# Optimization experiments

Hardware: AMD Instinct MI355X
Metric: run time of the kernel (lower is better)

Reference implementation:

```python
import jax, jax.numpy as jnp
import numpy as np

B, S, I, H = 64, 2048, 256, 256


def setup_inputs() -> dict:
    key = jax.random.key(0)
    kx, k1, k2, k3, k4 = jax.random.split(key, 5)
    s = 1.0 / np.sqrt(H)  # torch nn.Linear default init bound
    return {
        "x": jax.random.normal(kx, (B, S, I), dtype=jnp.float32),
        "W_xh": jax.random.uniform(k1, (H, I), jnp.float32, -s, s),
        "b_xh": jax.random.uniform(k2, (H,), jnp.float32, -s, s),
        "W_hh": jax.random.uniform(k3, (H, H), jnp.float32, -s, s),
        "b_hh": jax.random.uniform(k4, (H,), jnp.float32, -s, s),
    }


def reference(x, W_xh, b_xh, W_hh, b_hh):
    # Elman RNN, recurrence=True, tanh activation.
    # Precompute input projection for all timesteps in one batched matmul: (B,S,H)
    xp = jnp.einsum('bsi,hi->bsh', x, W_xh) + b_xh
    h0 = jnp.zeros((x.shape[0], W_hh.shape[0]), dtype=x.dtype)

    def step(h, xt):  # h: (B,H), xt: (B,H) precomputed input term
        h = jnp.tanh(h @ W_hh.T + b_hh + xt)
        return h, h

    h_last, hs = jax.lax.scan(step, h0, jnp.swapaxes(xp, 0, 1))  # hs: (S,B,H)
    h_seq = jnp.swapaxes(hs, 0, 1)  # (B,S,H), matches torch permute(1,0,2)
    return h_seq, h_last[None]  # final hidden: (1,B,H)
```

## Files before the change

kernel.cpp:

```cpp
#include <hip/hip_runtime.h>
#include <cstdint>
#include <cstddef>

typedef _Float16 h2 __attribute__((ext_vector_type(2)));

#define S_LEN 2048
#define HDIM  256
#define BATCH 64

__device__ __forceinline__ float dot2f(h2 a, h2 b, float c) {
#if __has_builtin(__builtin_amdgcn_fdot2)
    return __builtin_amdgcn_fdot2(a, b, c, false);
#else
    return c + (float)a[0] * (float)b[0] + (float)a[1] * (float)b[1];
#endif
}

__device__ __forceinline__ float tanh_fast(float x) {
    return 1.0f - 2.0f / (__expf(2.0f * x) + 1.0f);
}

__global__ void __launch_bounds__(256) xp_gemm(
    const float* __restrict__ x, const float* __restrict__ Wxh,
    const float* __restrict__ bxh, float* __restrict__ out) {
    __shared__ float As[32][68];
    __shared__ float Bs[32][68];

    const int tid = threadIdx.x;
    const int tx = tid & 15;
    const int ty = tid >> 4;
    const size_t m0 = (size_t)blockIdx.x * 64;
    const int n0 = blockIdx.y * 64;

    const int r = tid >> 3;
    const int c = (tid & 7) * 4;

    float bj[4];
#pragma unroll
    for (int j = 0; j < 4; j++) bj[j] = bxh[n0 + tx * 4 + j];

    float acc[4][4] = {};

    for (int k0 = 0; k0 < 256; k0 += 32) {
        float4 a0 = *(const float4*)&x[(m0 + r) * 256 + k0 + c];
        float4 a1 = *(const float4*)&x[(m0 + r + 32) * 256 + k0 + c];
        float4 b0 = *(const float4*)&Wxh[(size_t)(n0 + r) * 256 + k0 + c];
        float4 b1 = *(const float4*)&Wxh[(size_t)(n0 + r + 32) * 256 + k0 + c];

        __syncthreads();
        As[c + 0][r] = a0.x; As[c + 1][r] = a0.y; As[c + 2][r] = a0.z; As[c + 3][r] = a0.w;
        As[c + 0][r + 32] = a1.x; As[c + 1][r + 32] = a1.y; As[c + 2][r + 32] = a1.z; As[c + 3][r + 32] = a1.w;
        Bs[c + 0][r] = b0.x; Bs[c + 1][r] = b0.y; Bs[c + 2][r] = b0.z; Bs[c + 3][r] = b0.w;
        Bs[c + 0][r + 32] = b1.x; Bs[c + 1][r + 32] = b1.y; Bs[c + 2][r + 32] = b1.z; Bs[c + 3][r + 32] = b1.w;
        __syncthreads();

#pragma unroll
        for (int kk = 0; kk < 32; kk++) {
            float4 av = *(const float4*)&As[kk][ty * 4];
            float4 bv = *(const float4*)&Bs[kk][tx * 4];
            float aa[4] = {av.x, av.y, av.z, av.w};
            float bb[4] = {bv.x, bv.y, bv.z, bv.w};
#pragma unroll
            for (int i = 0; i < 4; i++)
#pragma unroll
                for (int j = 0; j < 4; j++)
                    acc[i][j] = fmaf(aa[i], bb[j], acc[i][j]);
        }
    }

#pragma unroll
    for (int i = 0; i < 4; i++) {
        float4 o;
        o.x = acc[i][0] + bj[0];
        o.y = acc[i][1] + bj[1];
        o.z = acc[i][2] + bj[2];
        o.w = acc[i][3] + bj[3];
        *(float4*)&out[(m0 + ty * 4 + i) * 256 + n0 + tx * 4] = o;
    }
}

__global__ void __launch_bounds__(512) rnn_recur(
    const float* __restrict__ Whh, const float* __restrict__ bhh,
    float* __restrict__ out) {
    const int b = blockIdx.x;
    const int t = threadIdx.x;
    const int h = t >> 1;
    const int half = t & 1;

    h2 w[64];
    const float* wrow = Whh + (size_t)h * HDIM + half * 128;
#pragma unroll
    for (int j = 0; j < 32; j++) {
        float4 wv = *(const float4*)&wrow[4 * j];
        w[2 * j]     = h2{(_Float16)wv.x, (_Float16)wv.y};
        w[2 * j + 1] = h2{(_Float16)wv.z, (_Float16)wv.w};
    }
    const float bias = bhh[h];

    __shared__ __align__(16) _Float16 hbuf[2][HDIM];
    for (int i = t; i < HDIM; i += 512) hbuf[0][i] = (_Float16)0.f;
    __syncthreads();

    float* xprow = out + (size_t)b * S_LEN * HDIM;
    float* hlast = out + (size_t)BATCH * S_LEN * HDIM;

    int p = 0;
    float val = 0.f;
    for (int s = 0; s < S_LEN; s++) {
        float xpv = xprow[(size_t)s * HDIM + h];

        const float4* hp4 = (const float4*)&hbuf[p][half * 128];
        float a0 = 0.f, a1 = 0.f, a2 = 0.f, a3 = 0.f;
#pragma unroll
        for (int j = 0; j < 16; j++) {
            float4 vv = hp4[j];
            a0 = dot2f(w[4 * j + 0], __builtin_bit_cast(h2, vv.x), a0);
            a1 = dot2f(w[4 * j + 1], __builtin_bit_cast(h2, vv.y), a1);
            a2 = dot2f(w[4 * j + 2], __builtin_bit_cast(h2, vv.z), a2);
            a3 = dot2f(w[4 * j + 3], __builtin_bit_cast(h2, vv.w), a3);
        }
        float part = (a0 + a1) + (a2 + a3);
        part += __shfl_xor(part, 1);

        val = tanh_fast(part + bias + xpv);

        if (half) {
            xprow[(size_t)s * HDIM + h] = val;
        } else {
            hbuf[p ^ 1][h] = (_Float16)val;
        }
        p ^= 1;
        __syncthreads();
    }
    if (!half) hlast[b * HDIM + h] = val;
}

extern "C" void kernel_launch(void* const* d_in, const int* in_sizes, int n_in,
                              void* d_out, int out_size, void* d_ws, size_t ws_size,
                              hipStream_t stream) {
    const float* x   = (const float*)d_in[0];
    const float* Wxh = (const float*)d_in[1];
    const float* bxh = (const float*)d_in[2];
    const float* Whh = (const float*)d_in[3];
    const float* bhh = (const float*)d_in[4];
    float* out = (float*)d_out;

    dim3 gridA(131072 / 64, 256 / 64);
    xp_gemm<<<gridA, 256, 0, stream>>>(x, Wxh, bxh, out);
    rnn_recur<<<BATCH, 512, 0, stream>>>(Whh, bhh, out);
}
```

Baseline: 1.530 ms.

## Batch 16 sequences per workgroup and run the recurrence with MFMA

Replaces the per-sequence dot2 recurrence (64 workgroups, one batch row each) with an MFMA-based kernel. Each of 4 workgroups handles 16 batch rows and does the h·W_hh^T product with 16x16x32 f16 MFMAs, keeping the weights in registers. Input-projection values are prefetched two timesteps ahead to hide global-load latency on the serial chain. The grid shrinks to 4 workgroups, trading parallelism across CUs for matrix-core throughput; the serial chain per step may lengthen, since each step now covers 16 rows in one workgroup.

After: 2.262 ms. 47.8% more time.

```diff
diff --git a/kernel.cpp b/kernel.cpp
--- a/kernel.cpp
+++ b/kernel.cpp
@@ -2,22 +2,17 @@
 #include <cstdint>
 #include <cstddef>
 
-typedef _Float16 h2 __attribute__((ext_vector_type(2)));
+typedef _Float16 half8 __attribute__((ext_vector_type(8)));
+typedef float f32x4 __attribute__((ext_vector_type(4)));
 
 #define S_LEN 2048
 #define HDIM  256
 #define BATCH 64
-
-__device__ __forceinline__ float dot2f(h2 a, h2 b, float c) {
-#if __has_builtin(__builtin_amdgcn_fdot2)
-    return __builtin_amdgcn_fdot2(a, b, c, false);
-#else
-    return c + (float)a[0] * (float)b[0] + (float)a[1] * (float)b[1];
-#endif
-}
+#define LROW  264
 
 __device__ __forceinline__ float tanh_fast(float x) {
-    return 1.0f - 2.0f / (__expf(2.0f * x) + 1.0f);
+    float e = __expf(2.0f * x);
+    return 1.0f - 2.0f / (e + 1.0f);
 }
 
 __global__ void __launch_bounds__(256) xp_gemm(
@@ -79,60 +74,106 @@
     }
 }
 
-__global__ void __launch_bounds__(512) rnn_recur(
+__global__ void __launch_bounds__(512, 1) rnn_mfma(
     const float* __restrict__ Whh, const float* __restrict__ bhh,
     float* __restrict__ out) {
-    const int b = blockIdx.x;
+    const int wg = blockIdx.x;
     const int t = threadIdx.x;
-    const int h = t >> 1;
-    const int half = t & 1;
+    const int w = t >> 6;
+    const int l = t & 63;
+    const int c = l & 15;
+    const int g = l >> 4;
 
-    h2 w[64];
-    const float* wrow = Whh + (size_t)h * HDIM + half * 128;
+    const int n0 = w * 32 + c;
+
+    __shared__ _Float16 hls[2][16][LROW];
+
+    half8 wf[2][8];
 #pragma unroll
-    for (int j = 0; j < 32; j++) {
-        float4 wv = *(const float4*)&wrow[4 * j];
-        w[2 * j]     = h2{(_Float16)wv.x, (_Float16)wv.y};
-        w[2 * j + 1] = h2{(_Float16)wv.z, (_Float16)wv.w};
+    for (int nt = 0; nt < 2; nt++) {
+        const float* wr = Whh + (size_t)(n0 + nt * 16) * HDIM;
+#pragma unroll
+        for (int kt = 0; kt < 8; kt++) {
+            float4 u = *(const float4*)&wr[kt * 32 + 8 * g];
+            float4 v = *(const float4*)&wr[kt * 32 + 8 * g + 4];
+            half8 f;
+            f[0] = (_Float16)u.x; f[1] = (_Float16)u.y;
+            f[2] = (_Float16)u.z; f[3] = (_Float16)u.w;
+            f[4] = (_Float16)v.x; f[5] = (_Float16)v.y;
+            f[6] = (_Float16)v.z; f[7] = (_Float16)v.w;
+            wf[nt][kt] = f;
+        }
     }
-    const float bias = bhh[h];
+    const float b0 = bhh[n0];
+    const float b1 = bhh[n0 + 16];
 
-    __shared__ __align__(16) _Float16 hbuf[2][HDIM];
-    for (int i = t; i < HDIM; i += 512) hbuf[0][i] = (_Float16)0.f;
+    for (int i = t; i < 16 * LROW; i += 512) (&hls[0][0][0])[i] = (_Float16)0.f;
+
+    float* bb[4];
+#pragma unroll
+    for (int r = 0; r < 4; r++)
+        bb[r] = out + (size_t)(wg * 16 + 4 * g + r) * S_LEN * HDIM;
+    float* hl = out + (size_t)BATCH * S_LEN * HDIM;
+
+    f32x4 xA0, xA1, xB0, xB1;
+#pragma unroll
+    for (int r = 0; r < 4; r++) {
+        xA0[r] = bb[r][n0];
+        xA1[r] = bb[r][n0 + 16];
+        xB0[r] = bb[r][HDIM + n0];
+        xB1[r] = bb[r][HDIM + n0 + 16];
+    }
+
     __syncthreads();
 
-    float* xprow = out + (size_t)b * S_LEN * HDIM;
-    float* hlast = out + (size_t)BATCH * S_LEN * HDIM;
+    int p = 0;
+    auto phase = [&](int s, f32x4& xq0, f32x4& xq1) {
+        half8 af[8];
+#pragma unroll
+        for (int kt = 0; kt < 8; kt++)
+            af[kt] = *(const half8*)&hls[p][c][kt * 32 + 8 * g];
 
-    int p = 0;
-    float val = 0.f;
-    for (int s = 0; s < S_LEN; s++) {
-        float xpv = xprow[(size_t)s * HDIM + h];
+        f32x4 acc0, acc1;
+#pragma unroll
+        for (int r = 0; r < 4; r++) {
+            acc0[r] = xq0[r] + b0;
+            acc1[r] = xq1[r] + b1;
+        }
 
-        const float4* hp4 = (const float4*)&hbuf[p][half * 128];
-        float a0 = 0.f, a1 = 0.f, a2 = 0.f, a3 = 0.f;
+        const int sp = (s + 2 < S_LEN) ? s + 2 : S_LEN - 1;
 #pragma unroll
-        for (int j = 0; j < 16; j++) {
-            float4 vv = hp4[j];
-            a0 = dot2f(w[4 * j + 0], __builtin_bit_cast(h2, vv.x), a0);
-            a1 = dot2f(w[4 * j + 1], __builtin_bit_cast(h2, vv.y), a1);
-            a2 = dot2f(w[4 * j + 2], __builtin_bit_cast(h2, vv.z), a2);
-            a3 = dot2f(w[4 * j + 3], __builtin_bit_cast(h2, vv.w), a3);
+        for (int r = 0; r < 4; r++) {
+            xq0[r] = bb[r][(size_t)sp * HDIM + n0];
+            xq1[r] = bb[r][(size_t)sp * HDIM + n0 + 16];
         }
-        float part = (a0 + a1) + (a2 + a3);
-        part += __shfl_xor(part, 1);
 
-        val = tanh_fast(part + bias + xpv);
+#pragma unroll
+        for (int kt = 0; kt < 8; kt++) {
+            acc0 = __builtin_amdgcn_mfma_f32_16x16x32_f16(af[kt], wf[0][kt], acc0, 0, 0, 0);
+            acc1 = __builtin_amdgcn_mfma_f32_16x16x32_f16(af[kt], wf[1][kt], acc1, 0, 0, 0);
+        }
 
-        if (half) {
-            xprow[(size_t)s * HDIM + h] = val;
-        } else {
-            hbuf[p ^ 1][h] = (_Float16)val;
+#pragma unroll
+        for (int r = 0; r < 4; r++) {
+            float v0 = tanh_fast(acc0[r]);
+            float v1 = tanh_fast(acc1[r]);
+            bb[r][(size_t)s * HDIM + n0] = v0;
+            bb[r][(size_t)s * HDIM + n0 + 16] = v1;
+            hls[p ^ 1][4 * g + r][n0] = (_Float16)v0;
+            hls[p ^ 1][4 * g + r][n0 + 16] = (_Float16)v1;
+            if (s == S_LEN - 1) {
+                hl[(wg * 16 + 4 * g + r) * HDIM + n0] = v0;
+                hl[(wg * 16 + 4 * g + r) * HDIM + n0 + 16] = v1;
+            }
         }
         p ^= 1;
         __syncthreads();
+    };
+
+    for (int s = 0; s < S_LEN; s += 2) {
+        phase(s, xA0, xA1);
+        phase(s + 1, xB0, xB1);
     }
-    if (!half) hlast[b * HDIM + h] = val;
 }
 
 extern "C" void kernel_launch(void* const* d_in, const int* in_sizes, int n_in,
@@ -147,5 +188,5 @@
 
     dim3 gridA(131072 / 64, 256 / 64);
     xp_gemm<<<gridA, 256, 0, stream>>>(x, Wxh, bxh, out);
-    rnn_recur<<<BATCH, 512, 0, stream>>>(Whh, bhh, out);
+    rnn_mfma<<<4, 512, 0, stream>>>(Whh, bhh, out);
 }
```
